# Kernel tuning notes

Measured on AMD Instinct MI355X. Metric: run time of the kernel, lower is better.

The kernel has to match this reference:

```python
import jax, jax.numpy as jnp
import numpy as np

N, E = 30000, 300000          # nodes, edges
IN, HID, OUT, H = 128, 256, 64, 4  # feature dims, GAT heads
NEG_SLOPE = 0.2
BN_EPS = 1e-5


def setup_inputs() -> dict:
    key = jax.random.key(0)
    ks = jax.random.split(key, 18)
    rn = lambda k, sh, sc: (jax.random.normal(k, sh, jnp.float32) * sc)
    return {
        "x": rn(ks[0], (N, IN), 1.0),
        "edge_index": jax.random.randint(ks[1], (2, E), 0, N, dtype=jnp.int64),
        # SAGEConv 1: lin_l (aggregated neighbors, with bias) + lin_r (root)
        "W1l": rn(ks[2], (IN, HID), IN ** -0.5),
        "b1l": jnp.zeros((HID,), jnp.float32),
        "W1r": rn(ks[3], (IN, HID), IN ** -0.5),
        # SAGEConv 2
        "W2l": rn(ks[4], (HID, OUT), HID ** -0.5),
        "b2l": jnp.zeros((OUT,), jnp.float32),
        "W2r": rn(ks[5], (HID, OUT), HID ** -0.5),
        # BatchNorms
        "g1": jnp.ones((HID,), jnp.float32),
        "be1": jnp.zeros((HID,), jnp.float32),
        "g2": jnp.ones((OUT,), jnp.float32),
        "be2": jnp.zeros((OUT,), jnp.float32),
        # GATConv: heads=4, concat=False (mean over heads)
        "Wg": rn(ks[6], (OUT, H * OUT), OUT ** -0.5),
        "att_src": rn(ks[7], (H, OUT), OUT ** -0.5),
        "att_dst": rn(ks[8], (H, OUT), OUT ** -0.5),
        "bg": jnp.zeros((OUT,), jnp.float32),
    }


def _forward(x, W1l, b1l, W1r, W2l, b2l, W2r, g1, be1, g2, be2,
             Wg, att_src, att_dst, bg, edge_index):
    src, dst = edge_index[0], edge_index[1]

    def sage(x, Wl, bl, Wr):
        # PyG SAGEConv: lin_l(mean_{j in N(i)} x_j) + lin_r(x_i)
        msg = jax.ops.segment_sum(x[src], dst, num_segments=N)       # [N, D]
        deg = jax.ops.segment_sum(jnp.ones((E, 1), x.dtype), dst, num_segments=N)
        agg = msg / jnp.maximum(deg, 1.0)
        return agg @ Wl + bl + x @ Wr

    def bn(x, g, b):  # batch-statistics BatchNorm1d (training-mode math)
        mu = x.mean(0)
        var = x.var(0)
        return g * (x - mu) * jax.lax.rsqrt(var + BN_EPS) + b

    x = jax.nn.relu(bn(sage(x, W1l, b1l, W1r), g1, be1))   # [N, HID]
    x = jax.nn.relu(bn(sage(x, W2l, b2l, W2r), g2, be2))   # [N, OUT]

    # GATConv with default add_self_loops=True
    loop = jnp.arange(N, dtype=src.dtype)
    s2 = jnp.concatenate([src, loop])
    d2 = jnp.concatenate([dst, loop])
    xp = (x @ Wg).reshape(N, H, OUT)                       # [N, H, D]
    a_src = (xp * att_src).sum(-1)                         # [N, H]
    a_dst = (xp * att_dst).sum(-1)                         # [N, H]
    e = jax.nn.leaky_relu(a_src[s2] + a_dst[d2], NEG_SLOPE)  # [E+N, H]
    # segment softmax over incoming edges per target node
    m = jax.ops.segment_max(e, d2, num_segments=N)
    ee = jnp.exp(e - m[d2])
    denom = jax.ops.segment_sum(ee, d2, num_segments=N)
    alpha = ee / denom[d2]                                 # [E+N, H]
    out = jax.ops.segment_sum(alpha[:, :, None] * xp[s2], d2, num_segments=N)
    out = out.mean(axis=1) + bg                            # concat=False -> head mean
    out = jax.nn.relu(out)
    return out.mean(axis=0, keepdims=True)                 # [1, OUT]


def reference(x, edge_index, W1l, b1l, W1r, W2l, b2l, W2r,
              g1, be1, g2, be2, Wg, att_src, att_dst, bg):
    return _forward(x, W1l, b1l, W1r, W2l, b2l, W2r, g1, be1, g2, be2,
                    Wg, att_src, att_dst, bg, edge_index)
```

## Files before the change

### kernel.cpp

```cpp
#include <hip/hip_runtime.h>
#include <stdint.h>

#define N_NODES 30000
#define N_EDGES 300000
#define BN_EPS  1e-5f
#define NEG_SLOPE 0.2f

typedef __attribute__((ext_vector_type(8))) short          s16x8;
typedef __attribute__((ext_vector_type(8))) unsigned short u16x8;
typedef __attribute__((ext_vector_type(4))) float          f32x4;

__device__ __forceinline__ float b2f(unsigned int u) { return __uint_as_float(u << 16); }
__device__ __forceinline__ unsigned short f2b(float f) {
    unsigned int u = __float_as_uint(f);
    return (unsigned short)((u + 0x7fffu + ((u >> 16) & 1u)) >> 16);
}
__device__ __forceinline__ float lrelu(float a) { return fmaxf(a, NEG_SLOPE * a); }

__global__ void k_prep(int* __restrict__ cnt, float* __restrict__ stats, float* __restrict__ outz,
                       const float* __restrict__ x, unsigned short* __restrict__ xb,
                       const float* __restrict__ W1l, const float* __restrict__ W1r,
                       const float* __restrict__ W2l, const float* __restrict__ W2r,
                       const float* __restrict__ Wg,
                       unsigned short* __restrict__ t1l, unsigned short* __restrict__ t1r,
                       unsigned short* __restrict__ t2l, unsigned short* __restrict__ t2r,
                       unsigned short* __restrict__ btf,
                       const float* __restrict__ att_src, const float* __restrict__ att_dst,
                       float* __restrict__ vsrc, float* __restrict__ vdst) {
    int b = blockIdx.x, tid = threadIdx.x;
    if (b < 118) {
        int i = b * 256 + tid;
        if (i < N_NODES) cnt[i] = 0;
        if (i < 1344) stats[i] = 0.f;
        if (b == 0 && tid < 64) outz[tid] = 0.f;
    } else if (b < 1118) {
        for (int i = (b - 118) * 256 + tid; i < N_NODES * 128 / 4; i += 256000) {
            float4 v = ((const float4*)x)[i];
            unsigned int lo = f2b(v.x) | ((unsigned int)f2b(v.y) << 16);
            unsigned int hi = f2b(v.z) | ((unsigned int)f2b(v.w) << 16);
            ((uint2*)xb)[i] = make_uint2(lo, hi);
        }
    } else if (b < 1566) {
        int i = (b - 1118) * 256 + tid;
        if (i >= 114688) return;
        if (i >= 98304) {
            int j = i - 98304;
            int n = j >> 8, r = j & 255;
            int h = r >> 6, k = r & 63;
            btf[j] = f2b(Wg[k * 256 + h * 64 + n] * 0.25f);
            return;
        }
        const float* S; unsigned short* D; int K, NN, off;
        if (i < 32768)      { S = W1l; D = t1l; K = 128; NN = 256; off = 0; }
        else if (i < 65536) { S = W1r; D = t1r; K = 128; NN = 256; off = 32768; }
        else if (i < 81920) { S = W2l; D = t2l; K = 256; NN = 64;  off = 65536; }
        else                { S = W2r; D = t2r; K = 256; NN = 64;  off = 81920; }
        int j = i - off;
        int k = j / NN, n = j % NN;
        D[n * K + k] = f2b(S[j]);
    } else {
        int h = tid >> 6, k = tid & 63;
        float s = 0.f, d = 0.f;
        for (int dd = 0; dd < 64; ++dd) {
            float w = Wg[k * 256 + h * 64 + dd];
            s += w * att_src[h * 64 + dd];
            d += w * att_dst[h * 64 + dd];
        }
        vsrc[h * 64 + k] = s;
        vdst[h * 64 + k] = d;
    }
}

__global__ void k_count(const int* __restrict__ dst, int* __restrict__ cnt) {
    int e = blockIdx.x * 256 + threadIdx.x;
    if (e < N_EDGES) atomicAdd(&cnt[dst[e]], 1);
}

__global__ void k_scan1(const int* __restrict__ cnt, int* __restrict__ rowptr, int* __restrict__ bsums) {
    __shared__ int s[256];
    int tid = threadIdx.x;
    int idx = blockIdx.x * 256 + tid;
    int val = (idx < N_NODES) ? cnt[idx] : 0;
    s[tid] = val; __syncthreads();
    for (int o = 1; o < 256; o <<= 1) {
        int add = (tid >= o) ? s[tid - o] : 0;
        __syncthreads();
        s[tid] += add;
        __syncthreads();
    }
    if (idx < N_NODES) rowptr[idx] = s[tid] - val;
    if (tid == 255) bsums[blockIdx.x] = s[255];
}

__global__ void k_scan2(int* bsums, int nb) {
    __shared__ int s[128];
    int tid = threadIdx.x;
    int val = (tid < nb) ? bsums[tid] : 0;
    s[tid] = val; __syncthreads();
    for (int o = 1; o < 128; o <<= 1) {
        int add = (tid >= o) ? s[tid - o] : 0;
        __syncthreads();
        s[tid] += add;
        __syncthreads();
    }
    if (tid < nb) bsums[tid] = s[tid] - val;
}

__global__ void k_scan3(int* __restrict__ rowptr, const int* __restrict__ bsums, int* __restrict__ cnt) {
    int idx = blockIdx.x * 256 + threadIdx.x;
    if (idx < N_NODES) { rowptr[idx] += bsums[idx >> 8]; cnt[idx] = 0; }
    if (idx == 0) rowptr[N_NODES] = N_EDGES;
}

__global__ void k_fill(const int* __restrict__ srcA, const int* __restrict__ dstA,
                       const int* __restrict__ rowptr, int* __restrict__ cnt, int* __restrict__ col) {
    int e = blockIdx.x * 256 + threadIdx.x;
    if (e < N_EDGES) {
        int d = dstA[e];
        int pos = rowptr[d] + atomicAdd(&cnt[d], 1);
        col[pos] = srcA[e];
    }
}

__global__ void __launch_bounds__(256) k_sage_agg_b(const unsigned short* __restrict__ X,
                                                    const int* __restrict__ rowptr,
                                                    const int* __restrict__ col,
                                                    unsigned short* __restrict__ out) {
    int lane = threadIdx.x & 63;
    int i = (blockIdx.x << 2) + (threadIdx.x >> 6);
    if (i >= N_NODES) return;
    int b = rowptr[i], e = rowptr[i + 1];
    float aA0 = 0.f, aA1 = 0.f, aB0 = 0.f, aB1 = 0.f;
    int p = b;
    for (; p + 4 <= e; p += 4) {
        int j0 = col[p], j1 = col[p + 1], j2 = col[p + 2], j3 = col[p + 3];
        unsigned int v0 = *(const unsigned int*)(X + (size_t)j0 * 128 + lane * 2);
        unsigned int v1 = *(const unsigned int*)(X + (size_t)j1 * 128 + lane * 2);
        unsigned int v2 = *(const unsigned int*)(X + (size_t)j2 * 128 + lane * 2);
        unsigned int v3 = *(const unsigned int*)(X + (size_t)j3 * 128 + lane * 2);
        aA0 += b2f(v0 & 0xffffu) + b2f(v2 & 0xffffu);
        aA1 += b2f(v0 >> 16) + b2f(v2 >> 16);
        aB0 += b2f(v1 & 0xffffu) + b2f(v3 & 0xffffu);
        aB1 += b2f(v1 >> 16) + b2f(v3 >> 16);
    }
    for (; p < e; ++p) {
        int j = col[p];
        unsigned int v = *(const unsigned int*)(X + (size_t)j * 128 + lane * 2);
        aA0 += b2f(v & 0xffffu);
        aA1 += b2f(v >> 16);
    }
    float inv = 1.f / fmaxf((float)(e - b), 1.f);
    float r0 = (aA0 + aB0) * inv, r1 = (aA1 + aB1) * inv;
    *(unsigned int*)(out + (size_t)i * 128 + lane * 2) = f2b(r0) | ((unsigned int)f2b(r1) << 16);
}

template<bool BF16OUT, bool BN_A, bool STATS>
__global__ void __launch_bounds__(256) k_mgemm(const unsigned short* __restrict__ A1,
                                               const unsigned short* __restrict__ Bt1, int K1,
                                               const unsigned short* __restrict__ A2,
                                               const unsigned short* __restrict__ Bt2, int K2,
                                               const float* __restrict__ bias,
                                               void* __restrict__ Cv, unsigned short* __restrict__ Cv2,
                                               int M, int NN,
                                               const float* __restrict__ bnA,
                                               const float* __restrict__ bnB,
                                               float* __restrict__ stS, float* __restrict__ stQ) {
    __shared__ unsigned short As[64 * 32];
    __shared__ unsigned short Bs[64 * 32];
    int tid = threadIdx.x;
    int w = tid >> 6, l = tid & 63;
    int mBase = blockIdx.x * 64, nBase = blockIdx.y * 64;
    f32x4 acc[4] = {};

    auto lds_off = [](int row, int col_bf16) -> int {
        return (row * 64 + col_bf16 * 2) ^ ((row & 7) << 4);
    };
    int srow = tid >> 2;
    int schunk = (tid & 3) << 3;
    int s_w_off = lds_off(srow, schunk);
    int kgrp = (l >> 4) << 3;
    int a_off = lds_off(w * 16 + (l & 15), kgrp);
    int b_off[4];
    #pragma unroll
    for (int c = 0; c < 4; ++c) b_off[c] = lds_off(c * 16 + (l & 15), kgrp);

    for (int pair = 0; pair < 2; ++pair) {
        const unsigned short* A  = pair ? A2 : A1;
        const unsigned short* Bt = pair ? Bt2 : Bt1;
        int K = pair ? K2 : K1;
        if (K == 0) break;
        for (int k0 = 0; k0 < K; k0 += 32) {
            u16x8 av = {};
            int arow = mBase + srow;
            if (arow < M) {
                av = *(const u16x8*)&A[(size_t)arow * K + k0 + schunk];
                if constexpr (BN_A) {
                    const float* pa = &bnA[k0 + schunk];
                    const float* pb = &bnB[k0 + schunk];
                    #pragma unroll
                    for (int e2 = 0; e2 < 8; ++e2) {
                        float f = fmaxf(b2f(av[e2]) * pa[e2] + pb[e2], 0.f);
                        av[e2] = f2b(f);
                    }
                }
            }
            u16x8 bv = *(const u16x8*)&Bt[(size_t)(nBase + srow) * K + k0 + schunk];
            *(u16x8*)((char*)As + s_w_off) = av;
            *(u16x8*)((char*)Bs + s_w_off) = bv;
            __syncthreads();
            s16x8 a = *(const s16x8*)((const char*)As + a_off);
            #pragma unroll
            for (int c = 0; c < 4; ++c) {
                s16x8 bfr = *(const s16x8*)((const char*)Bs + b_off[c]);
                acc[c] = __builtin_amdgcn_mfma_f32_16x16x32_bf16(a, bfr, acc[c], 0, 0, 0);
            }
            __syncthreads();
        }
    }

    float* lst = (float*)As;
    if constexpr (STATS) {
        if (tid < 128) lst[tid] = 0.f;
        __syncthreads();
    }
    int colb = l & 15;
    int rbase = (l >> 4) << 2;
    #pragma unroll
    for (int c = 0; c < 4; ++c) {
        int gcol = nBase + c * 16 + colb;
        float bi = bias ? bias[gcol] : 0.f;
        float s_ = 0.f, q_ = 0.f;
        #pragma unroll
        for (int r = 0; r < 4; ++r) {
            int grow = mBase + w * 16 + rbase + r;
            if (grow < M) {
                float v = acc[c][r] + bi;
                if constexpr (BF16OUT) {
                    unsigned short v16 = f2b(v);
                    if (Cv2) {
                        if (gcol < 64) ((unsigned short*)Cv)[(size_t)grow * 64 + gcol] = v16;
                        else           Cv2[(size_t)grow * 64 + gcol - 64] = v16;
                    } else {
                        ((unsigned short*)Cv)[(size_t)grow * NN + gcol] = v16;
                    }
                } else {
                    ((float*)Cv)[(size_t)grow * NN + gcol] = v;
                }
                if constexpr (STATS) { s_ += v; q_ += v * v; }
            }
        }
        if constexpr (STATS) {
            s_ += __shfl_xor(s_, 16); s_ += __shfl_xor(s_, 32);
            q_ += __shfl_xor(q_, 16); q_ += __shfl_xor(q_, 32);
            if (l < 16) {
                atomicAdd(&lst[c * 16 + l], s_);
                atomicAdd(&lst[64 + c * 16 + l], q_);
            }
        }
    }
    if constexpr (STATS) {
        __syncthreads();
        if (tid < 64) {
            atomicAdd(&stS[nBase + tid], lst[tid]);
            atomicAdd(&stQ[nBase + tid], lst[64 + tid]);
        }
    }
}

__global__ void __launch_bounds__(256) k_mgemm_mean(const unsigned short* __restrict__ A,
                                                    const unsigned short* __restrict__ Bt,
                                                    const float* __restrict__ bg,
                                                    float* __restrict__ out, int M) {
    __shared__ unsigned short As[64 * 32];
    __shared__ unsigned short Bs[64 * 32];
    __shared__ float lds_cols[64];
    int tid = threadIdx.x;
    int w = tid >> 6, l = tid & 63;
    int mBase = blockIdx.x * 64;
    if (tid < 64) lds_cols[tid] = 0.f;
    f32x4 acc[4] = {};

    auto lds_off = [](int row, int col_bf16) -> int {
        return (row * 64 + col_bf16 * 2) ^ ((row & 7) << 4);
    };
    int srow = tid >> 2;
    int schunk = (tid & 3) << 3;
    int s_w_off = lds_off(srow, schunk);
    int kgrp = (l >> 4) << 3;
    int a_off = lds_off(w * 16 + (l & 15), kgrp);
    int b_off[4];
    #pragma unroll
    for (int c = 0; c < 4; ++c) b_off[c] = lds_off(c * 16 + (l & 15), kgrp);

    const int K = 256;
    for (int k0 = 0; k0 < K; k0 += 32) {
        u16x8 av = {};
        int arow = mBase + srow;
        if (arow < M) av = *(const u16x8*)&A[(size_t)arow * K + k0 + schunk];
        u16x8 bv = *(const u16x8*)&Bt[(size_t)srow * K + k0 + schunk];
        *(u16x8*)((char*)As + s_w_off) = av;
        *(u16x8*)((char*)Bs + s_w_off) = bv;
        __syncthreads();
        s16x8 a = *(const s16x8*)((const char*)As + a_off);
        #pragma unroll
        for (int c = 0; c < 4; ++c) {
            s16x8 bfr = *(const s16x8*)((const char*)Bs + b_off[c]);
            acc[c] = __builtin_amdgcn_mfma_f32_16x16x32_bf16(a, bfr, acc[c], 0, 0, 0);
        }
        __syncthreads();
    }

    int colb = l & 15;
    int rbase = (l >> 4) << 2;
    #pragma unroll
    for (int c = 0; c < 4; ++c) {
        int gcol = c * 16 + colb;
        float bi = bg[gcol];
        float sc = 0.f;
        #pragma unroll
        for (int r = 0; r < 4; ++r) {
            int grow = mBase + w * 16 + rbase + r;
            if (grow < M) sc += fmaxf(acc[c][r] + bi, 0.f);
        }
        sc += __shfl_xor(sc, 16);
        sc += __shfl_xor(sc, 32);
        if (l < 16) atomicAdd(&lds_cols[c * 16 + l], sc);
    }
    __syncthreads();
    if (tid < 64) atomicAdd(out + tid, lds_cols[tid] * (1.f / N_NODES));
}

template<int C>
__global__ void k_finstats(const float* __restrict__ sum, const float* __restrict__ sq,
                           const float* __restrict__ g, const float* __restrict__ be,
                           float* __restrict__ A, float* __restrict__ B) {
    int c = threadIdx.x;
    if (c < C) {
        float mu = sum[c] * (1.f / N_NODES);
        float var = sq[c] * (1.f / N_NODES) - mu * mu;
        float a = g[c] * rsqrtf(var + BN_EPS);
        A[c] = a;
        B[c] = be[c] - a * mu;
    }
}

__global__ void __launch_bounds__(256) k_sage_add(const unsigned short* __restrict__ z2,
                                                  const unsigned short* __restrict__ r2,
                                                  const int* __restrict__ rowptr,
                                                  const int* __restrict__ col,
                                                  const float* __restrict__ b2l,
                                                  float* __restrict__ h2,
                                                  float* __restrict__ stS, float* __restrict__ stQ) {
    __shared__ float ls[128];
    int tid = threadIdx.x;
    if (tid < 128) ls[tid] = 0.f;
    __syncthreads();
    int lane = tid & 63;
    int wid = tid >> 6;
    float bl = b2l[lane];
    float s_ = 0.f, q_ = 0.f;
    for (int i = blockIdx.x * 4 + wid; i < N_NODES; i += gridDim.x * 4) {
        int b = rowptr[i], e = rowptr[i + 1];
        float aA = 0.f, aB = 0.f;
        int p = b;
        for (; p + 4 <= e; p += 4) {
            int j0 = col[p], j1 = col[p + 1], j2 = col[p + 2], j3 = col[p + 3];
            float v0 = b2f(z2[(size_t)j0 * 64 + lane]);
            float v1 = b2f(z2[(size_t)j1 * 64 + lane]);
            float v2 = b2f(z2[(size_t)j2 * 64 + lane]);
            float v3 = b2f(z2[(size_t)j3 * 64 + lane]);
            aA += v0 + v2;
            aB += v1 + v3;
        }
        for (; p < e; ++p) aA += b2f(z2[(size_t)col[p] * 64 + lane]);
        float inv = 1.f / fmaxf((float)(e - b), 1.f);
        float v = (aA + aB) * inv + bl + b2f(r2[(size_t)i * 64 + lane]);
        h2[(size_t)i * 64 + lane] = v;
        s_ += v; q_ += v * v;
    }
    atomicAdd(&ls[lane], s_);
    atomicAdd(&ls[64 + lane], q_);
    __syncthreads();
    if (tid < 64) {
        atomicAdd(&stS[tid], ls[tid]);
        atomicAdd(&stQ[tid], ls[64 + tid]);
    }
}

__global__ void __launch_bounds__(256) k_attn2(const float* __restrict__ h2,
                                               const float* __restrict__ A2s,
                                               const float* __restrict__ B2s,
                                               const float* __restrict__ vsrc,
                                               const float* __restrict__ vdst,
                                               unsigned short* __restrict__ h2b,
                                               float* __restrict__ att) {
    int tid = threadIdx.x;
    int lane = tid & 63;
    int wid = tid >> 6;
    float a2 = A2s[lane], b2 = B2s[lane];
    float vs0 = vsrc[lane], vs1 = vsrc[64 + lane], vs2 = vsrc[128 + lane], vs3 = vsrc[192 + lane];
    float vd0 = vdst[lane], vd1 = vdst[64 + lane], vd2 = vdst[128 + lane], vd3 = vdst[192 + lane];
    for (int i = blockIdx.x * 4 + wid; i < N_NODES; i += gridDim.x * 4) {
        float v = fmaxf(h2[(size_t)i * 64 + lane] * a2 + b2, 0.f);
        h2b[(size_t)i * 64 + lane] = f2b(v);
        float s0 = v * vs0, s1 = v * vs1, s2 = v * vs2, s3 = v * vs3;
        float d0 = v * vd0, d1 = v * vd1, d2 = v * vd2, d3 = v * vd3;
        #pragma unroll
        for (int o = 32; o; o >>= 1) {
            s0 += __shfl_xor(s0, o); s1 += __shfl_xor(s1, o);
            s2 += __shfl_xor(s2, o); s3 += __shfl_xor(s3, o);
            d0 += __shfl_xor(d0, o); d1 += __shfl_xor(d1, o);
            d2 += __shfl_xor(d2, o); d3 += __shfl_xor(d3, o);
        }
        if (lane == 0) {
            float4* ap = (float4*)(att + (size_t)i * 8);
            ap[0] = make_float4(s0, s1, s2, s3);
            ap[1] = make_float4(d0, d1, d2, d3);
        }
    }
}

__global__ void __launch_bounds__(256) k_gat2(const unsigned short* __restrict__ h2b,
                                              const float* __restrict__ att,
                                              const int* __restrict__ rowptr,
                                              const int* __restrict__ col,
                                              unsigned short* __restrict__ oagg) {
    int tid = threadIdx.x;
    int lane = tid & 63;
    int gw = (blockIdx.x << 2) + (tid >> 6);
    int stride = gridDim.x << 2;
    for (int i = gw; i < N_NODES; i += stride) {
        int b = rowptr[i], e = rowptr[i + 1];
        float4 ai = *(const float4*)(att + (size_t)i * 8);
        float4 ad = *(const float4*)(att + (size_t)i * 8 + 4);
        float hv = b2f(h2b[(size_t)i * 64 + lane]);
        float w0 = __expf(lrelu(ai.x + ad.x));
        float w1 = __expf(lrelu(ai.y + ad.y));
        float w2 = __expf(lrelu(ai.z + ad.z));
        float w3 = __expf(lrelu(ai.w + ad.w));
        float s0 = w0, s1 = w1, s2 = w2, s3 = w3;
        float a0 = w0 * hv, a1 = w1 * hv, a2 = w2 * hv, a3 = w3 * hv;
        int p = b;
        for (; p + 2 <= e; p += 2) {
            int j0 = col[p], j1 = col[p + 1];
            float4 aj0 = *(const float4*)(att + (size_t)j0 * 8);
            float4 aj1 = *(const float4*)(att + (size_t)j1 * 8);
            float hj0 = b2f(h2b[(size_t)j0 * 64 + lane]);
            float hj1 = b2f(h2b[(size_t)j1 * 64 + lane]);
            float e00 = __expf(lrelu(aj0.x + ad.x));
            float e01 = __expf(lrelu(aj0.y + ad.y));
            float e02 = __expf(lrelu(aj0.z + ad.z));
            float e03 = __expf(lrelu(aj0.w + ad.w));
            float e10 = __expf(lrelu(aj1.x + ad.x));
            float e11 = __expf(lrelu(aj1.y + ad.y));
            float e12 = __expf(lrelu(aj1.z + ad.z));
            float e13 = __expf(lrelu(aj1.w + ad.w));
            s0 += e00 + e10; a0 = fmaf(e00, hj0, fmaf(e10, hj1, a0));
            s1 += e01 + e11; a1 = fmaf(e01, hj0, fmaf(e11, hj1, a1));
            s2 += e02 + e12; a2 = fmaf(e02, hj0, fmaf(e12, hj1, a2));
            s3 += e03 + e13; a3 = fmaf(e03, hj0, fmaf(e13, hj1, a3));
        }
        if (p < e) {
            int j = col[p];
            float4 aj = *(const float4*)(att + (size_t)j * 8);
            float hj = b2f(h2b[(size_t)j * 64 + lane]);
            float e0 = __expf(lrelu(aj.x + ad.x));
            float e1 = __expf(lrelu(aj.y + ad.y));
            float e2 = __expf(lrelu(aj.z + ad.z));
            float e3 = __expf(lrelu(aj.w + ad.w));
            s0 += e0; a0 = fmaf(e0, hj, a0);
            s1 += e1; a1 = fmaf(e1, hj, a1);
            s2 += e2; a2 = fmaf(e2, hj, a2);
            s3 += e3; a3 = fmaf(e3, hj, a3);
        }
        unsigned short* op = oagg + (size_t)i * 256 + lane;
        op[0]   = f2b(a0 / s0);
        op[64]  = f2b(a1 / s1);
        op[128] = f2b(a2 / s2);
        op[192] = f2b(a3 / s3);
    }
}

extern "C" void kernel_launch(void* const* d_in, const int* in_sizes, int n_in,
                              void* d_out, int out_size, void* d_ws, size_t ws_size,
                              hipStream_t stream) {
    const float* x       = (const float*)d_in[0];
    const int*   ei      = (const int*)d_in[1];
    const float* W1l     = (const float*)d_in[2];
    const float* b1l     = (const float*)d_in[3];
    const float* W1r     = (const float*)d_in[4];
    const float* W2l     = (const float*)d_in[5];
    const float* b2l     = (const float*)d_in[6];
    const float* W2r     = (const float*)d_in[7];
    const float* g1      = (const float*)d_in[8];
    const float* be1     = (const float*)d_in[9];
    const float* g2      = (const float*)d_in[10];
    const float* be2     = (const float*)d_in[11];
    const float* Wg      = (const float*)d_in[12];
    const float* att_src = (const float*)d_in[13];
    const float* att_dst = (const float*)d_in[14];
    const float* bg      = (const float*)d_in[15];
    float* out = (float*)d_out;

    char* p = (char*)d_ws;
    auto alloc = [&](size_t bytes) -> char* {
        char* q = p;
        p += (bytes + 255) & ~(size_t)255;
        return q;
    };
    int*   cnt    = (int*)alloc((size_t)N_NODES * 4);
    float* stats  = (float*)alloc(1856 * 4);
    int*   rowptr = (int*)alloc((size_t)(N_NODES + 1) * 4);
    int*   bsums  = (int*)alloc(256 * 4);
    int*   col    = (int*)alloc((size_t)N_EDGES * 4);
    unsigned short* xb    = (unsigned short*)alloc((size_t)N_NODES * 128 * 2);
    unsigned short* agg1b = (unsigned short*)alloc((size_t)N_NODES * 128 * 2);
    unsigned short* h1b = (unsigned short*)alloc((size_t)N_NODES * 256 * 2);
    float* h2   = (float*)alloc((size_t)N_NODES * 64 * 4);
    unsigned short* h2b = (unsigned short*)alloc((size_t)N_NODES * 64 * 2);
    float* att  = (float*)alloc((size_t)N_NODES * 8 * 4);
    unsigned short* w1lt = (unsigned short*)alloc(128 * 256 * 2);
    unsigned short* w1rt = (unsigned short*)alloc(128 * 256 * 2);
    unsigned short* w2lt = (unsigned short*)alloc(256 * 64 * 2);
    unsigned short* w2rt = (unsigned short*)alloc(256 * 64 * 2);
    unsigned short* btf  = (unsigned short*)alloc(64 * 256 * 2);

    unsigned short* z2 = agg1b;
    unsigned short* r2 = agg1b + (size_t)N_NODES * 64;
    unsigned short* oagg = xb;

    float* sum1 = stats;        float* sq1 = stats + 256;
    float* A1s  = stats + 512;  float* B1s = stats + 768;
    float* sum2 = stats + 1024; float* sq2 = stats + 1088;
    float* A2s  = stats + 1152; float* B2s = stats + 1216;
    float* vsrc = stats + 1344; float* vdst = stats + 1600;

    const int* srcA = ei;
    const int* dstA = ei + N_EDGES;

    k_prep<<<1567, 256, 0, stream>>>(cnt, stats, out, x, xb, W1l, W1r, W2l, W2r, Wg,
                                     w1lt, w1rt, w2lt, w2rt, btf, att_src, att_dst, vsrc, vdst);
    k_count<<<1172, 256, 0, stream>>>(dstA, cnt);
    k_scan1<<<118, 256, 0, stream>>>(cnt, rowptr, bsums);
    k_scan2<<<1, 128, 0, stream>>>(bsums, 118);
    k_scan3<<<118, 256, 0, stream>>>(rowptr, bsums, cnt);
    k_fill<<<1172, 256, 0, stream>>>(srcA, dstA, rowptr, cnt, col);

    k_sage_agg_b<<<7500, 256, 0, stream>>>(xb, rowptr, col, agg1b);
    k_mgemm<true, false, true><<<dim3(469, 4), 256, 0, stream>>>(
        agg1b, w1lt, 128, xb, w1rt, 128, b1l, h1b, nullptr, N_NODES, 256, nullptr, nullptr, sum1, sq1);
    k_finstats<256><<<1, 256, 0, stream>>>(sum1, sq1, g1, be1, A1s, B1s);

    k_mgemm<true, true, false><<<dim3(469, 2), 256, 0, stream>>>(
        h1b, w2lt, 256, nullptr, nullptr, 0, nullptr, z2, r2, N_NODES, 128, A1s, B1s, nullptr, nullptr);
    k_sage_add<<<1875, 256, 0, stream>>>(z2, r2, rowptr, col, b2l, h2, sum2, sq2);
    k_finstats<64><<<1, 64, 0, stream>>>(sum2, sq2, g2, be2, A2s, B2s);

    k_attn2<<<1875, 256, 0, stream>>>(h2, A2s, B2s, vsrc, vdst, h2b, att);
    k_gat2<<<2048, 256, 0, stream>>>(h2b, att, rowptr, col, oagg);
    k_mgemm_mean<<<469, 256, 0, stream>>>(oagg, btf, bg, out, N_NODES);
}
```

Baseline: 245.5 us.

## Add cache warm-up kernels, split SAGE aggregation by halves, fold BN stats and scan

Adds prefetch kernels that stream gather tables (xb halves, z2, h2b+att) into the last-level cache before each irregular gather kernel. The first SAGE aggregation is split into two passes over 64-column halves so each working set is smaller. The separate finstats and scan2 kernels are removed by computing BN coefficients inside the consuming kernels and doing the block-sum scan redundantly in scan3. Streaming col, output and intermediate accesses are switched to nontemporal loads and stores. This trades extra launches and redundant reads for fewer cache misses during the gathers.

```diff
diff --git a/kernel.cpp b/kernel.cpp
--- a/kernel.cpp
+++ b/kernel.cpp
@@ -16,6 +16,33 @@
     return (unsigned short)((u + 0x7fffu + ((u >> 16) & 1u)) >> 16);
 }
 __device__ __forceinline__ float lrelu(float a) { return fmaxf(a, NEG_SLOPE * a); }
+
+__global__ void __launch_bounds__(256) k_warm2(const uint4* __restrict__ p1, int n1,
+                                               const uint4* __restrict__ p2, int n2,
+                                               unsigned int* __restrict__ sink) {
+    int s = blockIdx.x >> 3;
+    unsigned int a = 0;
+    for (int i = s * 256 + threadIdx.x; i < n1; i += 16384) {
+        uint4 v = p1[i]; a ^= v.x ^ v.y ^ v.z ^ v.w;
+    }
+    if (p2)
+        for (int i = s * 256 + threadIdx.x; i < n2; i += 16384) {
+            uint4 v = p2[i]; a ^= v.x ^ v.y ^ v.z ^ v.w;
+        }
+    sink[blockIdx.x] = a;
+}
+
+__global__ void __launch_bounds__(256) k_warm_h(const uint4* __restrict__ p, int q,
+                                                unsigned int* __restrict__ sink) {
+    int s = blockIdx.x >> 3;
+    unsigned int a = 0;
+    for (int i = s * 256 + threadIdx.x; i < 240000; i += 16384) {
+        int r = i >> 3, c = i & 7;
+        uint4 v = p[r * 16 + q * 8 + c];
+        a ^= v.x ^ v.y ^ v.z ^ v.w;
+    }
+    sink[blockIdx.x] = a;
+}
 
 __global__ void k_prep(int* __restrict__ cnt, float* __restrict__ stats, float* __restrict__ outz,
                        const float* __restrict__ x, unsigned short* __restrict__ xb,
@@ -92,23 +119,20 @@
     if (tid == 255) bsums[blockIdx.x] = s[255];
 }
 
-__global__ void k_scan2(int* bsums, int nb) {
-    __shared__ int s[128];
-    int tid = threadIdx.x;
-    int val = (tid < nb) ? bsums[tid] : 0;
-    s[tid] = val; __syncthreads();
+__global__ void k_scan3(int* __restrict__ rowptr, const int* __restrict__ bsums, int* __restrict__ cnt) {
+    __shared__ int ls[128];
+    int tid = threadIdx.x;
+    if (tid < 128) ls[tid] = (tid < 118) ? bsums[tid] : 0;
+    __syncthreads();
     for (int o = 1; o < 128; o <<= 1) {
-        int add = (tid >= o) ? s[tid - o] : 0;
-        __syncthreads();
-        s[tid] += add;
-        __syncthreads();
-    }
-    if (tid < nb) bsums[tid] = s[tid] - val;
-}
-
-__global__ void k_scan3(int* __restrict__ rowptr, const int* __restrict__ bsums, int* __restrict__ cnt) {
-    int idx = blockIdx.x * 256 + threadIdx.x;
-    if (idx < N_NODES) { rowptr[idx] += bsums[idx >> 8]; cnt[idx] = 0; }
+        int add = (tid < 128 && tid >= o) ? ls[tid - o] : 0;
+        __syncthreads();
+        if (tid < 128) ls[tid] += add;
+        __syncthreads();
+    }
+    int ex = (blockIdx.x == 0) ? 0 : ls[blockIdx.x - 1];
+    int idx = blockIdx.x * 256 + tid;
+    if (idx < N_NODES) { rowptr[idx] += ex; cnt[idx] = 0; }
     if (idx == 0) rowptr[N_NODES] = N_EDGES;
 }
 
@@ -122,36 +146,33 @@
     }
 }
 
-__global__ void __launch_bounds__(256) k_sage_agg_b(const unsigned short* __restrict__ X,
+__global__ void __launch_bounds__(256) k_sage_agg_h(const unsigned short* __restrict__ X,
                                                     const int* __restrict__ rowptr,
                                                     const int* __restrict__ col,
-                                                    unsigned short* __restrict__ out) {
+                                                    unsigned short* __restrict__ out, int q) {
     int lane = threadIdx.x & 63;
     int i = (blockIdx.x << 2) + (threadIdx.x >> 6);
     if (i >= N_NODES) return;
     int b = rowptr[i], e = rowptr[i + 1];
-    float aA0 = 0.f, aA1 = 0.f, aB0 = 0.f, aB1 = 0.f;
+    int base = q * 64 + lane;
+    float aA = 0.f, aB = 0.f, aC = 0.f, aD = 0.f;
     int p = b;
     for (; p + 4 <= e; p += 4) {
-        int j0 = col[p], j1 = col[p + 1], j2 = col[p + 2], j3 = col[p + 3];
-        unsigned int v0 = *(const unsigned int*)(X + (size_t)j0 * 128 + lane * 2);
-        unsigned int v1 = *(const unsigned int*)(X + (size_t)j1 * 128 + lane * 2);
-        unsigned int v2 = *(const unsigned int*)(X + (size_t)j2 * 128 + lane * 2);
-        unsigned int v3 = *(const unsigned int*)(X + (size_t)j3 * 128 + lane * 2);
-        aA0 += b2f(v0 & 0xffffu) + b2f(v2 & 0xffffu);
-        aA1 += b2f(v0 >> 16) + b2f(v2 >> 16);
-        aB0 += b2f(v1 & 0xffffu) + b2f(v3 & 0xffffu);
-        aB1 += b2f(v1 >> 16) + b2f(v3 >> 16);
+        int j0 = __builtin_nontemporal_load(col + p);
+        int j1 = __builtin_nontemporal_load(col + p + 1);
+        int j2 = __builtin_nontemporal_load(col + p + 2);
+        int j3 = __builtin_nontemporal_load(col + p + 3);
+        aA += b2f(X[(size_t)j0 * 128 + base]);
+        aB += b2f(X[(size_t)j1 * 128 + base]);
+        aC += b2f(X[(size_t)j2 * 128 + base]);
+        aD += b2f(X[(size_t)j3 * 128 + base]);
     }
     for (; p < e; ++p) {
-        int j = col[p];
-        unsigned int v = *(const unsigned int*)(X + (size_t)j * 128 + lane * 2);
-        aA0 += b2f(v & 0xffffu);
-        aA1 += b2f(v >> 16);
+        int j = __builtin_nontemporal_load(col + p);
+        aA += b2f(X[(size_t)j * 128 + base]);
     }
     float inv = 1.f / fmaxf((float)(e - b), 1.f);
-    float r0 = (aA0 + aB0) * inv, r1 = (aA1 + aB1) * inv;
-    *(unsigned int*)(out + (size_t)i * 128 + lane * 2) = f2b(r0) | ((unsigned int)f2b(r1) << 16);
+    __builtin_nontemporal_store(f2b((aA + aB + aC + aD) * inv), &out[(size_t)i * 128 + base]);
 }
 
 template<bool BF16OUT, bool BN_A, bool STATS>
@@ -162,15 +183,27 @@
                                                const float* __restrict__ bias,
                                                void* __restrict__ Cv, unsigned short* __restrict__ Cv2,
                                                int M, int NN,
-                                               const float* __restrict__ bnA,
-                                               const float* __restrict__ bnB,
+                                               const float* __restrict__ bn_sum,
+                                               const float* __restrict__ bn_sq,
+                                               const float* __restrict__ bn_g,
+                                               const float* __restrict__ bn_be,
                                                float* __restrict__ stS, float* __restrict__ stQ) {
     __shared__ unsigned short As[64 * 32];
     __shared__ unsigned short Bs[64 * 32];
+    __shared__ float bnAl[256], bnBl[256];
     int tid = threadIdx.x;
     int w = tid >> 6, l = tid & 63;
     int mBase = blockIdx.x * 64, nBase = blockIdx.y * 64;
     f32x4 acc[4] = {};
+
+    if constexpr (BN_A) {
+        float mu = bn_sum[tid] * (1.f / N_NODES);
+        float var = bn_sq[tid] * (1.f / N_NODES) - mu * mu;
+        float a = bn_g[tid] * rsqrtf(var + BN_EPS);
+        bnAl[tid] = a;
+        bnBl[tid] = bn_be[tid] - a * mu;
+        __syncthreads();
+    }
 
     auto lds_off = [](int row, int col_bf16) -> int {
         return (row * 64 + col_bf16 * 2) ^ ((row & 7) << 4);
@@ -195,8 +228,8 @@
             if (arow < M) {
                 av = *(const u16x8*)&A[(size_t)arow * K + k0 + schunk];
                 if constexpr (BN_A) {
-                    const float* pa = &bnA[k0 + schunk];
-                    const float* pb = &bnB[k0 + schunk];
+                    const float* pa = &bnAl[k0 + schunk];
+                    const float* pb = &bnBl[k0 + schunk];
                     #pragma unroll
                     for (int e2 = 0; e2 < 8; ++e2) {
                         float f = fmaxf(b2f(av[e2]) * pa[e2] + pb[e2], 0.f);
@@ -330,20 +363,6 @@
     if (tid < 64) atomicAdd(out + tid, lds_cols[tid] * (1.f / N_NODES));
 }
 
-template<int C>
-__global__ void k_finstats(const float* __restrict__ sum, const float* __restrict__ sq,
-                           const float* __restrict__ g, const float* __restrict__ be,
-                           float* __restrict__ A, float* __restrict__ B) {
-    int c = threadIdx.x;
-    if (c < C) {
-        float mu = sum[c] * (1.f / N_NODES);
-        float var = sq[c] * (1.f / N_NODES) - mu * mu;
-        float a = g[c] * rsqrtf(var + BN_EPS);
-        A[c] = a;
-        B[c] = be[c] - a * mu;
-    }
-}
-
 __global__ void __launch_bounds__(256) k_sage_add(const unsigned short* __restrict__ z2,
                                                   const unsigned short* __restrict__ r2,
                                                   const int* __restrict__ rowptr,
@@ -364,7 +383,10 @@
         float aA = 0.f, aB = 0.f;
         int p = b;
         for (; p + 4 <= e; p += 4) {
-            int j0 = col[p], j1 = col[p + 1], j2 = col[p + 2], j3 = col[p + 3];
+            int j0 = __builtin_nontemporal_load(col + p);
+            int j1 = __builtin_nontemporal_load(col + p + 1);
+            int j2 = __builtin_nontemporal_load(col + p + 2);
+            int j3 = __builtin_nontemporal_load(col + p + 3);
             float v0 = b2f(z2[(size_t)j0 * 64 + lane]);
             float v1 = b2f(z2[(size_t)j1 * 64 + lane]);
             float v2 = b2f(z2[(size_t)j2 * 64 + lane]);
@@ -372,10 +394,10 @@
             aA += v0 + v2;
             aB += v1 + v3;
         }
-        for (; p < e; ++p) aA += b2f(z2[(size_t)col[p] * 64 + lane]);
+        for (; p < e; ++p) aA += b2f(z2[(size_t)__builtin_nontemporal_load(col + p) * 64 + lane]);
         float inv = 1.f / fmaxf((float)(e - b), 1.f);
-        float v = (aA + aB) * inv + bl + b2f(r2[(size_t)i * 64 + lane]);
-        h2[(size_t)i * 64 + lane] = v;
+        float v = (aA + aB) * inv + bl + b2f(__builtin_nontemporal_load(r2 + (size_t)i * 64 + lane));
+        __builtin_nontemporal_store(v, &h2[(size_t)i * 64 + lane]);
         s_ += v; q_ += v * v;
     }
     atomicAdd(&ls[lane], s_);
@@ -388,8 +410,10 @@
 }
 
 __global__ void __launch_bounds__(256) k_attn2(const float* __restrict__ h2,
-                                               const float* __restrict__ A2s,
-                                               const float* __restrict__ B2s,
+                                               const float* __restrict__ sum2,
+                                               const float* __restrict__ sq2,
+                                               const float* __restrict__ g2,
+                                               const float* __restrict__ be2,
                                                const float* __restrict__ vsrc,
                                                const float* __restrict__ vdst,
                                                unsigned short* __restrict__ h2b,
@@ -397,11 +421,14 @@
     int tid = threadIdx.x;
     int lane = tid & 63;
     int wid = tid >> 6;
-    float a2 = A2s[lane], b2 = B2s[lane];
+    float mu = sum2[lane] * (1.f / N_NODES);
+    float var = sq2[lane] * (1.f / N_NODES) - mu * mu;
+    float a2 = g2[lane] * rsqrtf(var + BN_EPS);
+    float b2v = be2[lane] - a2 * mu;
     float vs0 = vsrc[lane], vs1 = vsrc[64 + lane], vs2 = vsrc[128 + lane], vs3 = vsrc[192 + lane];
     float vd0 = vdst[lane], vd1 = vdst[64 + lane], vd2 = vdst[128 + lane], vd3 = vdst[192 + lane];
     for (int i = blockIdx.x * 4 + wid; i < N_NODES; i += gridDim.x * 4) {
-        float v = fmaxf(h2[(size_t)i * 64 + lane] * a2 + b2, 0.f);
+        float v = fmaxf(__builtin_nontemporal_load(h2 + (size_t)i * 64 + lane) * a2 + b2v, 0.f);
         h2b[(size_t)i * 64 + lane] = f2b(v);
         float s0 = v * vs0, s1 = v * vs1, s2 = v * vs2, s3 = v * vs3;
         float d0 = v * vd0, d1 = v * vd1, d2 = v * vd2, d3 = v * vd3;
@@ -442,7 +469,8 @@
         float a0 = w0 * hv, a1 = w1 * hv, a2 = w2 * hv, a3 = w3 * hv;
         int p = b;
         for (; p + 2 <= e; p += 2) {
-            int j0 = col[p], j1 = col[p + 1];
+            int j0 = __builtin_nontemporal_load(col + p);
+            int j1 = __builtin_nontemporal_load(col + p + 1);
             float4 aj0 = *(const float4*)(att + (size_t)j0 * 8);
             float4 aj1 = *(const float4*)(att + (size_t)j1 * 8);
             float hj0 = b2f(h2b[(size_t)j0 * 64 + lane]);
@@ -461,7 +489,7 @@
             s3 += e03 + e13; a3 = fmaf(e03, hj0, fmaf(e13, hj1, a3));
         }
         if (p < e) {
-            int j = col[p];
+            int j = __builtin_nontemporal_load(col + p);
             float4 aj = *(const float4*)(att + (size_t)j * 8);
             float hj = b2f(h2b[(size_t)j * 64 + lane]);
             float e0 = __expf(lrelu(aj.x + ad.x));
@@ -474,10 +502,10 @@
             s3 += e3; a3 = fmaf(e3, hj, a3);
         }
         unsigned short* op = oagg + (size_t)i * 256 + lane;
-        op[0]   = f2b(a0 / s0);
-        op[64]  = f2b(a1 / s1);
-        op[128] = f2b(a2 / s2);
-        op[192] = f2b(a3 / s3);
+        __builtin_nontemporal_store(f2b(a0 / s0), op);
+        __builtin_nontemporal_store(f2b(a1 / s1), op + 64);
+        __builtin_nontemporal_store(f2b(a2 / s2), op + 128);
+        __builtin_nontemporal_store(f2b(a3 / s3), op + 192);
     }
 }
 
@@ -512,6 +540,7 @@
     float* stats  = (float*)alloc(1856 * 4);
     int*   rowptr = (int*)alloc((size_t)(N_NODES + 1) * 4);
     int*   bsums  = (int*)alloc(256 * 4);
+    unsigned int* wsink = (unsigned int*)alloc(512 * 4);
     int*   col    = (int*)alloc((size_t)N_EDGES * 4);
     unsigned short* xb    = (unsigned short*)alloc((size_t)N_NODES * 128 * 2);
     unsigned short* agg1b = (unsigned short*)alloc((size_t)N_NODES * 128 * 2);
@@ -530,9 +559,7 @@
     unsigned short* oagg = xb;
 
     float* sum1 = stats;        float* sq1 = stats + 256;
-    float* A1s  = stats + 512;  float* B1s = stats + 768;
     float* sum2 = stats + 1024; float* sq2 = stats + 1088;
-    float* A2s  = stats + 1152; float* B2s = stats + 1216;
     float* vsrc = stats + 1344; float* vdst = stats + 1600;
 
     const int* srcA = ei;
@@ -542,21 +569,25 @@
                                      w1lt, w1rt, w2lt, w2rt, btf, att_src, att_dst, vsrc, vdst);
     k_count<<<1172, 256, 0, stream>>>(dstA, cnt);
     k_scan1<<<118, 256, 0, stream>>>(cnt, rowptr, bsums);
-    k_scan2<<<1, 128, 0, stream>>>(bsums, 118);
     k_scan3<<<118, 256, 0, stream>>>(rowptr, bsums, cnt);
     k_fill<<<1172, 256, 0, stream>>>(srcA, dstA, rowptr, cnt, col);
 
-    k_sage_agg_b<<<7500, 256, 0, stream>>>(xb, rowptr, col, agg1b);
+    k_warm_h<<<512, 256, 0, stream>>>((const uint4*)xb, 0, wsink);
+    k_sage_agg_h<<<7500, 256, 0, stream>>>(xb, rowptr, col, agg1b, 0);
+    k_warm_h<<<512, 256, 0, stream>>>((const uint4*)xb, 1, wsink);
+    k_sage_agg_h<<<7500, 256, 0, stream>>>(xb, rowptr, col, agg1b, 1);
     k_mgemm<true, false, true><<<dim3(469, 4), 256, 0, stream>>>(
-        agg1b, w1lt, 128, xb, w1rt, 128, b1l, h1b, nullptr, N_NODES, 256, nullptr, nullptr, sum1, sq1);
-    k_finstats<256><<<1, 256, 0, stream>>>(sum1, sq1, g1, be1, A1s, B1s);
+        agg1b, w1lt, 128, xb, w1rt, 128, b1l, h1b, nullptr, N_NODES, 256,
+        nullptr, nullptr, nullptr, nullptr, sum1, sq1);
 
     k_mgemm<true, true, false><<<dim3(469, 2), 256, 0, stream>>>(
-        h1b, w2lt, 256, nullptr, nullptr, 0, nullptr, z2, r2, N_NODES, 128, A1s, B1s, nullptr, nullptr);
+        h1b, w2lt, 256, nullptr, nullptr, 0, nullptr, z2, r2, N_NODES, 128,
+        sum1, sq1, g1, be1, nullptr, nullptr);
+    k_warm2<<<512, 256, 0, stream>>>((const uint4*)z2, 240000, nullptr, 0, wsink);
     k_sage_add<<<1875, 256, 0, stream>>>(z2, r2, rowptr, col, b2l, h2, sum2, sq2);
-    k_finstats<64><<<1, 64, 0, stream>>>(sum2, sq2, g2, be2, A2s, B2s);
-
-    k_attn2<<<1875, 256, 0, stream>>>(h2, A2s, B2s, vsrc, vdst, h2b, att);
+
+    k_attn2<<<1875, 256, 0, stream>>>(h2, sum2, sq2, g2, be2, vsrc, vdst, h2b, att);
+    k_warm2<<<512, 256, 0, stream>>>((const uint4*)h2b, 240000, (const uint4*)att, 60000, wsink);
     k_gat2<<<2048, 256, 0, stream>>>(h2b, att, rowptr, col, oagg);
     k_mgemm_mean<<<469, 256, 0, stream>>>(oagg, btf, bg, out, N_NODES);
 }
```

After: 283.4 us. +15.4%, slower.
